# Optimization experiments

Hardware: AMD Instinct MI355X
Metric: run time of the kernel (lower is better)

## Reference

```python
import jax, jax.numpy as jnp
import numpy as np

N_NODES = 50000
N_EDGES = 800000
D_IN = 64
F1 = 64
F2 = 64
D_HID = 100


def setup_inputs() -> dict:
    key = jax.random.key(0)
    ks = jax.random.split(key, 12)
    x = jax.random.normal(ks[0], (N_NODES, D_IN), dtype=jnp.float32)
    edge_src = jax.random.randint(ks[1], (N_EDGES,), 0, N_NODES, dtype=jnp.int32)
    edge_dst = jax.random.randint(ks[2], (N_EDGES,), 0, N_NODES, dtype=jnp.int32)
    # stands in for pre-normalized GCN adjacency values (D^-1/2 (A+I) D^-1/2)
    edge_weight = jax.random.uniform(ks[3], (N_EDGES,), dtype=jnp.float32)
    def glorot(k, shape):
        lim = np.sqrt(6.0 / (shape[0] + shape[1]))
        return jax.random.uniform(k, shape, jnp.float32, -lim, lim)
    W1 = glorot(ks[4], (D_IN, F1))
    b1 = jnp.zeros((F1,), jnp.float32)
    W2 = glorot(ks[5], (F1, F2))
    b2 = jnp.zeros((F2,), jnp.float32)
    Wd = glorot(ks[6], (F2, D_HID))
    bd = jnp.zeros((D_HID,), jnp.float32)
    Wo = glorot(ks[7], (D_HID, 1))
    bo = jnp.zeros((1,), jnp.float32)
    return {"x": x, "edge_src": edge_src, "edge_dst": edge_dst,
            "edge_weight": edge_weight, "W1": W1, "b1": b1, "W2": W2,
            "b2": b2, "Wd": Wd, "bd": bd, "Wo": Wo, "bo": bo}


def _gcn_conv(x, edge_src, edge_dst, edge_weight, W, b):
    # spektral GCNConv: out = swish(A_norm @ (X @ W) + b)
    h = x @ W                                        # [N, F]
    msg = h[edge_src] * edge_weight[:, None]          # [E, F] gather + scale
    agg = jax.ops.segment_sum(msg, edge_dst, num_segments=N_NODES)  # [N, F]
    return jax.nn.swish(agg + b)


def reference(x, edge_src, edge_dst, edge_weight, W1, b1, W2, b2, Wd, bd, Wo, bo):
    h = _gcn_conv(x, edge_src, edge_dst, edge_weight, W1, b1)
    h = _gcn_conv(h, edge_src, edge_dst, edge_weight, W2, b2)
    h = jax.nn.swish(h @ Wd + bd)                    # Dense(100, swish)
    return jax.nn.sigmoid(h @ Wo + bo)               # Dense(1, sigmoid) -> [N, 1]
```

## Files before the change

### kernel.cpp

```cpp
#include <hip/hip_runtime.h>
#include <hip/hip_fp16.h>

#define N_NODES 50000
#define N_EDGES 800000
#define D 64
#define DHID 100
#define NTILES (N_NODES / 16)
#define NCT 7
#define CAP 32
#define SPILL_MAX 8192
#define NGROUPS 4
#define NSLICES 780
#define FILL_BLOCKS (NGROUPS * NSLICES)
#define MM_BLOCKS ((NTILES + 3) / 4)
#define DST_PER_GROUP (N_NODES / NGROUPS)
#define FSTRIDE (NSLICES * 256)
#define KMAX 5

typedef unsigned short ushort;
typedef unsigned int uint;
typedef __attribute__((ext_vector_type(8))) short s16x8;
typedef __attribute__((ext_vector_type(4))) float f32x4;

#define MFMA16(A, B, C) __builtin_amdgcn_mfma_f32_16x16x32_bf16((A), (B), (C), 0, 0, 0)

__device__ __forceinline__ float swishf(float x) { return x / (1.0f + __expf(-x)); }

__device__ __forceinline__ ushort f2bf(float f) {
    uint u = __float_as_uint(f);
    uint r = (u + 0x7fffu + ((u >> 16) & 1u)) >> 16;
    return (ushort)r;
}
__device__ __forceinline__ float bf2f(ushort h) { return __uint_as_float((uint)h << 16); }
__device__ __forceinline__ float bf_lo(uint d) { return __uint_as_float(d << 16); }
__device__ __forceinline__ float bf_hi(uint d) { return __uint_as_float(d & 0xffff0000u); }

__device__ __forceinline__ float hwf(uint e) {
    return __half2float(__ushort_as_half((ushort)(e >> 16)));
}

__device__ __forceinline__ void accum8(float* acc, uint4 v, float w) {
    acc[0] = fmaf(w, bf_lo(v.x), acc[0]);
    acc[1] = fmaf(w, bf_hi(v.x), acc[1]);
    acc[2] = fmaf(w, bf_lo(v.y), acc[2]);
    acc[3] = fmaf(w, bf_hi(v.y), acc[3]);
    acc[4] = fmaf(w, bf_lo(v.z), acc[4]);
    acc[5] = fmaf(w, bf_hi(v.z), acc[5]);
    acc[6] = fmaf(w, bf_lo(v.w), acc[6]);
    acc[7] = fmaf(w, bf_hi(v.w), acc[7]);
}

__device__ __forceinline__ void gather_body(const ushort* __restrict__ H,
                                            uint4 eA, uint4 eB, int degv,
                                            int j, int fg, float* acc) {
#pragma unroll
    for (int t = 0; t < 8; ++t) acc[t] = 0.f;
    const int sA = j * 4, sB = 16 + j * 4;
    bool pA = sA < degv, pB = sB < degv;
    uint4 vA0, vA1, vA2, vA3, vB0, vB1, vB2, vB3;
    float wA0 = 0, wA1 = 0, wA2 = 0, wA3 = 0;
    float wB0 = 0, wB1 = 0, wB2 = 0, wB3 = 0;
    if (pA) {
        wA0 = hwf(eA.x);
        wA1 = (sA + 1 < degv) ? hwf(eA.y) : 0.f;
        wA2 = (sA + 2 < degv) ? hwf(eA.z) : 0.f;
        wA3 = (sA + 3 < degv) ? hwf(eA.w) : 0.f;
        uint i0 = min(eA.x & 0xffffu, (uint)(N_NODES - 1));
        uint i1 = min(eA.y & 0xffffu, (uint)(N_NODES - 1));
        uint i2 = min(eA.z & 0xffffu, (uint)(N_NODES - 1));
        uint i3 = min(eA.w & 0xffffu, (uint)(N_NODES - 1));
        vA0 = *((const uint4*)(H + ((size_t)i0 << 6) + (fg << 3)));
        vA1 = *((const uint4*)(H + ((size_t)i1 << 6) + (fg << 3)));
        vA2 = *((const uint4*)(H + ((size_t)i2 << 6) + (fg << 3)));
        vA3 = *((const uint4*)(H + ((size_t)i3 << 6) + (fg << 3)));
    }
    if (pB) {
        wB0 = hwf(eB.x);
        wB1 = (sB + 1 < degv) ? hwf(eB.y) : 0.f;
        wB2 = (sB + 2 < degv) ? hwf(eB.z) : 0.f;
        wB3 = (sB + 3 < degv) ? hwf(eB.w) : 0.f;
        uint i0 = min(eB.x & 0xffffu, (uint)(N_NODES - 1));
        uint i1 = min(eB.y & 0xffffu, (uint)(N_NODES - 1));
        uint i2 = min(eB.z & 0xffffu, (uint)(N_NODES - 1));
        uint i3 = min(eB.w & 0xffffu, (uint)(N_NODES - 1));
        vB0 = *((const uint4*)(H + ((size_t)i0 << 6) + (fg << 3)));
        vB1 = *((const uint4*)(H + ((size_t)i1 << 6) + (fg << 3)));
        vB2 = *((const uint4*)(H + ((size_t)i2 << 6) + (fg << 3)));
        vB3 = *((const uint4*)(H + ((size_t)i3 << 6) + (fg << 3)));
    }
    if (pA) {
        accum8(acc, vA0, wA0);
        accum8(acc, vA1, wA1);
        accum8(acc, vA2, wA2);
        accum8(acc, vA3, wA3);
    }
    if (pB) {
        accum8(acc, vB0, wB0);
        accum8(acc, vB1, wB1);
        accum8(acc, vB2, wB2);
        accum8(acc, vB3, wB3);
    }
#pragma unroll
    for (int t = 0; t < 8; ++t) {
        acc[t] += __shfl_xor(acc[t], 8, 64);
        acc[t] += __shfl_xor(acc[t], 16, 64);
    }
}

__device__ __forceinline__ void add_spills(const ushort* __restrict__ H,
                                           const int* __restrict__ spillCnt,
                                           const uint2* __restrict__ spill,
                                           int node, int fg, float* acc) {
    int n = min(*spillCnt, SPILL_MAX);
    for (int i = 0; i < n; ++i) {
        uint2 sp = spill[i];
        if ((int)sp.x == node) {
            float wv = hwf(sp.y);
            uint si = min(sp.y & 0xffffu, (uint)(N_NODES - 1));
            uint4 v = *((const uint4*)(H + ((size_t)si << 6) + (fg << 3)));
            accum8(acc, v, wv);
        }
    }
}

__global__ __launch_bounds__(256) void fill_and_l1(const int* __restrict__ src,
                                                   const int* __restrict__ dst,
                                                   const float* __restrict__ w,
                                                   int* __restrict__ deg,
                                                   uint* __restrict__ csr,
                                                   int* __restrict__ spillCnt,
                                                   uint2* __restrict__ spill,
                                                   const float* __restrict__ X,
                                                   const float* __restrict__ W,
                                                   const float* __restrict__ W2,
                                                   const float* __restrict__ Wd,
                                                   short* __restrict__ W2T2,
                                                   short* __restrict__ WdT2,
                                                   ushort* __restrict__ H) {
    __shared__ __align__(16) short sBT[2][D][72];
    int tid = threadIdx.x;

    if (blockIdx.x < FILL_BLOCKS) {
        const int g = blockIdx.x & (NGROUPS - 1);
        const int s = blockIdx.x >> 2;
        const int lo = g * DST_PER_GROUP;
        const int e0 = s * 256 + tid;
        int d[KMAX];
        bool mk[KMAX];
#pragma unroll
        for (int k = 0; k < KMAX; ++k) {
            int e = e0 + k * FSTRIDE;
            int dv = (e < N_EDGES) ? dst[e] : -1;
            d[k] = dv;
            mk[k] = ((uint)(dv - lo) < (uint)DST_PER_GROUP);
        }
        float wv5[KMAX];
        int sv5[KMAX];
#pragma unroll
        for (int k = 0; k < KMAX; ++k)
            if (mk[k]) {
                int e = e0 + k * FSTRIDE;
                wv5[k] = __builtin_nontemporal_load(w + e);
                sv5[k] = __builtin_nontemporal_load(src + e);
            }
        int r5[KMAX];
#pragma unroll
        for (int k = 0; k < KMAX; ++k)
            if (mk[k]) r5[k] = atomicAdd(&deg[d[k]], 1);
#pragma unroll
        for (int k = 0; k < KMAX; ++k)
            if (mk[k]) {
                uint hw = (uint)__half_as_ushort(__float2half_rn(wv5[k]));
                uint payload = (uint)sv5[k] | (hw << 16);
                int r = r5[k];
                if (r < CAP) {
                    csr[(d[k] << 5) + r] = payload;
                } else {
                    int si = atomicAdd(spillCnt, 1);
                    if (si < SPILL_MAX) spill[si] = make_uint2((uint)d[k], payload);
                }
            }
        return;
    }

    if (blockIdx.x >= FILL_BLOCKS + MM_BLOCKS) {
        if (blockIdx.x == FILL_BLOCKS + MM_BLOCKS) {
            for (int idx = tid; idx < D * D; idx += 256) {
                int k = idx >> 6, c = idx & 63;
                float wv = W2[idx];
                ushort hi = f2bf(wv);
                W2T2[(size_t)c * D + k] = (short)hi;
                W2T2[(size_t)(D + c) * D + k] = (short)f2bf(wv - bf2f(hi));
            }
        } else {
            for (int idx = tid; idx < NCT * 16 * D; idx += 256) {
                int jj = idx >> 6, k = idx & 63;
                float wv = (jj < DHID) ? Wd[k * DHID + jj] : 0.f;
                ushort hi = f2bf(wv);
                WdT2[(size_t)jj * D + k] = (short)hi;
                WdT2[(size_t)(NCT * 16 + jj) * D + k] = (short)f2bf(wv - bf2f(hi));
            }
        }
        return;
    }

    for (int idx = tid; idx < D * D; idx += 256) {
        int k = idx >> 6, c = idx & 63;
        float wv = W[idx];
        ushort hi = f2bf(wv);
        sBT[0][c][k] = (short)hi;
        sBT[1][c][k] = (short)f2bf(wv - bf2f(hi));
    }
    __syncthreads();
    int wv_ = tid >> 6, lane = tid & 63, quad = lane >> 4, m = lane & 15;
    int tile = min((blockIdx.x - FILL_BLOCKS) * 4 + wv_, NTILES - 1);
    int node0 = tile * 16;

    f32x4 acc[4] = {{0,0,0,0},{0,0,0,0},{0,0,0,0},{0,0,0,0}};
#pragma unroll
    for (int kt = 0; kt < 2; ++kt) {
        int k0 = kt * 32 + quad * 8;
        const float* xp = X + ((size_t)(node0 + m) << 6) + k0;
        f32x4 xa = __builtin_nontemporal_load((const f32x4*)xp);
        f32x4 xb = __builtin_nontemporal_load((const f32x4*)(xp + 4));
        float xv[8] = {xa[0], xa[1], xa[2], xa[3], xb[0], xb[1], xb[2], xb[3]};
        s16x8 ahi, alo;
#pragma unroll
        for (int jj = 0; jj < 8; ++jj) {
            ushort hi = f2bf(xv[jj]);
            ahi[jj] = (short)hi;
            alo[jj] = (short)f2bf(xv[jj] - bf2f(hi));
        }
#pragma unroll
        for (int ct = 0; ct < 4; ++ct) {
            int n = ct * 16 + m;
            s16x8 bhi = *((const s16x8*)&sBT[0][n][k0]);
            s16x8 blo = *((const s16x8*)&sBT[1][n][k0]);
            acc[ct] = MFMA16(ahi, bhi, acc[ct]);
            acc[ct] = MFMA16(ahi, blo, acc[ct]);
            acc[ct] = MFMA16(alo, bhi, acc[ct]);
        }
    }
    __syncthreads();
    short (*rep)[16][72] = (short(*)[16][72])&sBT[0][0][0];
#pragma unroll
    for (int ct = 0; ct < 4; ++ct)
#pragma unroll
        for (int r = 0; r < 4; ++r)
            rep[wv_][quad * 4 + r][ct * 16 + m] = (short)f2bf(acc[ct][r]);
#pragma unroll
    for (int half = 0; half < 2; ++half) {
        int r = (lane >> 3) + half * 8;
        int c0 = (lane & 7) * 8;
        s16x8 v = *((const s16x8*)&rep[wv_][r][c0]);
        *((s16x8*)(H + ((size_t)(node0 + r) << 6) + c0)) = v;
    }
}

__global__ __launch_bounds__(256) void gather_act(const ushort* __restrict__ H,
                                                  const int* __restrict__ deg,
                                                  const uint* __restrict__ csr,
                                                  const int* __restrict__ spillCnt,
                                                  const uint2* __restrict__ spill,
                                                  const float* __restrict__ bias,
                                                  ushort* __restrict__ actOut) {
    int tid = threadIdx.x;
    int wave = tid >> 6, lane = tid & 63;
    int h = lane >> 5, j = (lane >> 3) & 3, fg = lane & 7;
    int node = blockIdx.x * 8 + wave * 2 + h;
    const uint* bucket = csr + ((size_t)node << 5);
    uint4 eA = *((const uint4*)(bucket + j * 4));
    uint4 eB = *((const uint4*)(bucket + 16 + j * 4));
    int degv = min(deg[node], CAP);

    float acc[8];
    gather_body(H, eA, eB, degv, j, fg, acc);
    if (j == 0) {
        add_spills(H, spillCnt, spill, node, fg, acc);
        float4 ba = ((const float4*)bias)[fg * 2];
        float4 bb = ((const float4*)bias)[fg * 2 + 1];
        float r0 = swishf(acc[0] + ba.x);
        float r1 = swishf(acc[1] + ba.y);
        float r2 = swishf(acc[2] + ba.z);
        float r3 = swishf(acc[3] + ba.w);
        float r4 = swishf(acc[4] + bb.x);
        float r5 = swishf(acc[5] + bb.y);
        float r6 = swishf(acc[6] + bb.z);
        float r7 = swishf(acc[7] + bb.w);
        uint4 u;
        u.x = (uint)f2bf(r0) | ((uint)f2bf(r1) << 16);
        u.y = (uint)f2bf(r2) | ((uint)f2bf(r3) << 16);
        u.z = (uint)f2bf(r4) | ((uint)f2bf(r5) << 16);
        u.w = (uint)f2bf(r6) | ((uint)f2bf(r7) << 16);
        *((uint4*)(actOut + ((size_t)node << 6) + (fg << 3))) = u;
    }
}

__global__ __launch_bounds__(256) void gather_tail(const ushort* __restrict__ act1,
                                                   const int* __restrict__ deg,
                                                   const uint* __restrict__ csr,
                                                   const int* __restrict__ spillCnt,
                                                   const uint2* __restrict__ spill,
                                                   const short* __restrict__ W2T2,
                                                   const float* __restrict__ b2,
                                                   const short* __restrict__ WdT2,
                                                   const float* __restrict__ bd,
                                                   const float* __restrict__ Wo,
                                                   const float* __restrict__ bo,
                                                   float* __restrict__ out) {
    __shared__ __align__(16) float sAgg[16][72];
    __shared__ __align__(16) short sAct2[16][72];
    __shared__ float sPart[4][16];
    int tid = threadIdx.x;
    int wv = tid >> 6, lane = tid & 63;
    int h = lane >> 5, j = (lane >> 3) & 3, fg = lane & 7;
    int quad = lane >> 4, m = lane & 15;
    int node0 = blockIdx.x * 16;

    {
        int n0l = wv * 4 + h, n1l = wv * 4 + 2 + h;
        int n0 = node0 + n0l, n1 = node0 + n1l;
        const uint* b0 = csr + ((size_t)n0 << 5);
        const uint* b1 = csr + ((size_t)n1 << 5);
        uint4 eA0 = *((const uint4*)(b0 + j * 4));
        uint4 eB0 = *((const uint4*)(b0 + 16 + j * 4));
        uint4 eA1 = *((const uint4*)(b1 + j * 4));
        uint4 eB1 = *((const uint4*)(b1 + 16 + j * 4));
        int d0 = min(deg[n0], CAP);
        int d1 = min(deg[n1], CAP);

        float acc0[8];
        gather_body(act1, eA0, eB0, d0, j, fg, acc0);
        if (j == 0) {
            add_spills(act1, spillCnt, spill, n0, fg, acc0);
            float4 u0 = {acc0[0], acc0[1], acc0[2], acc0[3]};
            float4 u1 = {acc0[4], acc0[5], acc0[6], acc0[7]};
            *((float4*)&sAgg[n0l][fg * 8]) = u0;
            *((float4*)&sAgg[n0l][fg * 8 + 4]) = u1;
        }
        float acc1[8];
        gather_body(act1, eA1, eB1, d1, j, fg, acc1);
        if (j == 0) {
            add_spills(act1, spillCnt, spill, n1, fg, acc1);
            float4 u0 = {acc1[0], acc1[1], acc1[2], acc1[3]};
            float4 u1 = {acc1[4], acc1[5], acc1[6], acc1[7]};
            *((float4*)&sAgg[n1l][fg * 8]) = u0;
            *((float4*)&sAgg[n1l][fg * 8 + 4]) = u1;
        }
    }
    __syncthreads();

    {
        f32x4 acc = {0, 0, 0, 0};
        int n = wv * 16 + m;
#pragma unroll
        for (int kt = 0; kt < 2; ++kt) {
            int k0 = kt * 32 + quad * 8;
            float4 xa = *((const float4*)&sAgg[m][k0]);
            float4 xb = *((const float4*)&sAgg[m][k0 + 4]);
            float xv[8] = {xa.x, xa.y, xa.z, xa.w, xb.x, xb.y, xb.z, xb.w};
            s16x8 ahi, alo;
#pragma unroll
            for (int jj = 0; jj < 8; ++jj) {
                ushort hi = f2bf(xv[jj]);
                ahi[jj] = (short)hi;
                alo[jj] = (short)f2bf(xv[jj] - bf2f(hi));
            }
            s16x8 bhi = *((const s16x8*)(W2T2 + (size_t)n * D + k0));
            s16x8 blo = *((const s16x8*)(W2T2 + (size_t)(D + n) * D + k0));
            acc = MFMA16(ahi, bhi, acc);
            acc = MFMA16(ahi, blo, acc);
            acc = MFMA16(alo, bhi, acc);
        }
        float bv = b2[n];
#pragma unroll
        for (int r = 0; r < 4; ++r)
            sAct2[quad * 4 + r][n] = (short)f2bf(swishf(acc[r] + bv));
    }
    __syncthreads();

    float part[4] = {0, 0, 0, 0};
#pragma unroll
    for (int cc = 0; cc < 2; ++cc) {
        int ct = wv + cc * 4;
        if (ct < NCT) {
            f32x4 acc = {0, 0, 0, 0};
            int n = ct * 16 + m;
#pragma unroll
            for (int kt = 0; kt < 2; ++kt) {
                int k0 = kt * 32 + quad * 8;
                s16x8 a = *((const s16x8*)&sAct2[m][k0]);
                s16x8 bhi = *((const s16x8*)(WdT2 + (size_t)n * D + k0));
                s16x8 blo = *((const s16x8*)(WdT2 + (size_t)(NCT * 16 + n) * D + k0));
                acc = MFMA16(a, bhi, acc);
                acc = MFMA16(a, blo, acc);
            }
            float bdv = (n < DHID) ? bd[n] : 0.f;
            float wov = (n < DHID) ? Wo[n] : 0.f;
#pragma unroll
            for (int r = 0; r < 4; ++r)
                part[r] = fmaf(swishf(acc[r] + bdv), wov, part[r]);
        }
    }
#pragma unroll
    for (int r = 0; r < 4; ++r) {
        part[r] += __shfl_xor(part[r], 1, 64);
        part[r] += __shfl_xor(part[r], 2, 64);
        part[r] += __shfl_xor(part[r], 4, 64);
        part[r] += __shfl_xor(part[r], 8, 64);
    }
    if (m == 0) {
#pragma unroll
        for (int r = 0; r < 4; ++r)
            sPart[wv][quad * 4 + r] = part[r];
    }
    __syncthreads();
    if (tid < 16) {
        float z = sPart[0][tid] + sPart[1][tid] + sPart[2][tid] + sPart[3][tid] + bo[0];
        out[node0 + tid] = 1.f / (1.f + __expf(-z));
    }
}

extern "C" void kernel_launch(void* const* d_in, const int* in_sizes, int n_in,
                              void* d_out, int out_size, void* d_ws, size_t ws_size,
                              hipStream_t stream) {
    const float* x   = (const float*)d_in[0];
    const int* esrc  = (const int*)d_in[1];
    const int* edst  = (const int*)d_in[2];
    const float* ew  = (const float*)d_in[3];
    const float* W1  = (const float*)d_in[4];
    const float* b1  = (const float*)d_in[5];
    const float* W2  = (const float*)d_in[6];
    const float* b2  = (const float*)d_in[7];
    const float* Wd  = (const float*)d_in[8];
    const float* bd  = (const float*)d_in[9];
    const float* Wo  = (const float*)d_in[10];
    const float* bo  = (const float*)d_in[11];
    float* out = (float*)d_out;

    char* ws = (char*)d_ws;
    ushort* H1    = (ushort*)ws; ws += (size_t)N_NODES * D * sizeof(ushort);
    ushort* act1  = (ushort*)ws; ws += (size_t)N_NODES * D * sizeof(ushort);
    uint* csr     = (uint*)ws;   ws += (size_t)N_NODES * CAP * sizeof(uint);
    int* deg      = (int*)ws;    ws += (size_t)N_NODES * sizeof(int);
    int* spillCnt = (int*)ws;    ws += 4 * sizeof(int);
    uint2* spill  = (uint2*)ws;  ws += (size_t)SPILL_MAX * sizeof(uint2);
    short* W2T2   = (short*)ws;  ws += (size_t)2 * D * D * sizeof(short);
    short* WdT2   = (short*)ws;  ws += (size_t)2 * NCT * 16 * D * sizeof(short);

    const int gBlocks = N_NODES / 8;

    hipMemsetAsync(deg, 0, (size_t)(N_NODES + 4) * sizeof(int), stream);

    fill_and_l1<<<FILL_BLOCKS + MM_BLOCKS + 2, 256, 0, stream>>>(
        esrc, edst, ew, deg, csr, spillCnt, spill, x, W1, W2, Wd, W2T2, WdT2, H1);

    gather_act<<<gBlocks, 256, 0, stream>>>(H1, deg, csr, spillCnt, spill, b1, act1);

    gather_tail<<<NTILES, 256, 0, stream>>>(act1, deg, csr, spillCnt, spill,
                                            W2T2, b2, WdT2, bd, Wo, bo, out);
}
```

Baseline: 179.7 us.

## Fuse three kernels into one persistent kernel with software grid barriers

Replaces the fill/L1, gather_act and gather_tail launches with one persistent kernel of 768 blocks. The phases are separated by atomic-counter grid barriers, and work is spread with grid-stride loops. This removes two kernel launch gaps and the tail effects between stages. In exchange, fewer blocks cover the scatter and gather phases, barrier spin cost is added, and correctness depends on all 768 blocks being resident at once.

```diff
diff --git a/kernel.cpp b/kernel.cpp
--- a/kernel.cpp
+++ b/kernel.cpp
@@ -10,12 +10,14 @@
 #define CAP 32
 #define SPILL_MAX 8192
 #define NGROUPS 4
-#define NSLICES 780
-#define FILL_BLOCKS (NGROUPS * NSLICES)
-#define MM_BLOCKS ((NTILES + 3) / 4)
 #define DST_PER_GROUP (N_NODES / NGROUPS)
-#define FSTRIDE (NSLICES * 256)
-#define KMAX 5
+#define NBLK 768
+#define NTHR 256
+#define GSIZE (NBLK * NTHR)
+#define FILLB 512
+#define L1B (NBLK - FILLB)
+#define FILL_NSL (FILLB / NGROUPS)
+#define FILL_STRIDE (FILL_NSL * NTHR)
 
 typedef unsigned short ushort;
 typedef unsigned int uint;
@@ -48,6 +50,28 @@
     acc[5] = fmaf(w, bf_hi(v.z), acc[5]);
     acc[6] = fmaf(w, bf_lo(v.w), acc[6]);
     acc[7] = fmaf(w, bf_hi(v.w), acc[7]);
+}
+
+struct GBar { uint cnt; uint gen; };
+
+__device__ __forceinline__ void gbar(GBar* b) {
+    __syncthreads();
+    if (threadIdx.x == 0) {
+        __threadfence();
+        uint g = atomicAdd(&b->gen, 0u);
+        uint v = atomicAdd(&b->cnt, 1u) + 1;
+        if (v == (uint)NBLK) {
+            atomicAdd(&b->gen, 1u);
+        } else {
+            int t = 0;
+            while (atomicAdd(&b->gen, 0u) == g) {
+                __builtin_amdgcn_s_sleep(8);
+                if (++t > 1000000) break;
+            }
+        }
+        __threadfence();
+    }
+    __syncthreads();
 }
 
 __device__ __forceinline__ void gather_body(const ushort* __restrict__ H,
@@ -123,301 +147,270 @@
     }
 }
 
-__global__ __launch_bounds__(256) void fill_and_l1(const int* __restrict__ src,
-                                                   const int* __restrict__ dst,
-                                                   const float* __restrict__ w,
-                                                   int* __restrict__ deg,
-                                                   uint* __restrict__ csr,
-                                                   int* __restrict__ spillCnt,
-                                                   uint2* __restrict__ spill,
-                                                   const float* __restrict__ X,
-                                                   const float* __restrict__ W,
-                                                   const float* __restrict__ W2,
-                                                   const float* __restrict__ Wd,
-                                                   short* __restrict__ W2T2,
-                                                   short* __restrict__ WdT2,
-                                                   ushort* __restrict__ H) {
+__global__ __launch_bounds__(NTHR, 4) void mega(const int* __restrict__ src,
+                                                const int* __restrict__ dst,
+                                                const float* __restrict__ w,
+                                                const float* __restrict__ X,
+                                                const float* __restrict__ W1,
+                                                const float* __restrict__ b1,
+                                                const float* __restrict__ W2,
+                                                const float* __restrict__ b2,
+                                                const float* __restrict__ Wd,
+                                                const float* __restrict__ bd,
+                                                const float* __restrict__ Wo,
+                                                const float* __restrict__ bo,
+                                                float* __restrict__ out,
+                                                int* __restrict__ deg,
+                                                uint* __restrict__ csr,
+                                                uint2* __restrict__ spill,
+                                                ushort* __restrict__ H1,
+                                                ushort* __restrict__ act1,
+                                                short* __restrict__ W2T2,
+                                                short* __restrict__ WdT2) {
     __shared__ __align__(16) short sBT[2][D][72];
-    int tid = threadIdx.x;
-
-    if (blockIdx.x < FILL_BLOCKS) {
-        const int g = blockIdx.x & (NGROUPS - 1);
-        const int s = blockIdx.x >> 2;
+    __shared__ __align__(16) char smemB[9216];
+    const int tid = threadIdx.x;
+    const int bid = blockIdx.x;
+    const int gtid = bid * NTHR + tid;
+    int* spillCnt = deg + N_NODES;
+    GBar* gb = (GBar*)(deg + N_NODES + 2);
+
+    for (int idx = gtid; idx < D * D; idx += GSIZE) {
+        int k = idx >> 6, c = idx & 63;
+        float wv = W2[idx];
+        ushort hi = f2bf(wv);
+        W2T2[(size_t)c * D + k] = (short)hi;
+        W2T2[(size_t)(D + c) * D + k] = (short)f2bf(wv - bf2f(hi));
+    }
+    for (int idx = gtid; idx < NCT * 16 * D; idx += GSIZE) {
+        int jj = idx >> 6, k = idx & 63;
+        float wv = (jj < DHID) ? Wd[k * DHID + jj] : 0.f;
+        ushort hi = f2bf(wv);
+        WdT2[(size_t)jj * D + k] = (short)hi;
+        WdT2[(size_t)(NCT * 16 + jj) * D + k] = (short)f2bf(wv - bf2f(hi));
+    }
+
+    if (bid < FILLB) {
+        const int g = bid & (NGROUPS - 1);
+        const int s = bid >> 2;
         const int lo = g * DST_PER_GROUP;
-        const int e0 = s * 256 + tid;
-        int d[KMAX];
-        bool mk[KMAX];
-#pragma unroll
-        for (int k = 0; k < KMAX; ++k) {
-            int e = e0 + k * FSTRIDE;
-            int dv = (e < N_EDGES) ? dst[e] : -1;
-            d[k] = dv;
-            mk[k] = ((uint)(dv - lo) < (uint)DST_PER_GROUP);
-        }
-        float wv5[KMAX];
-        int sv5[KMAX];
-#pragma unroll
-        for (int k = 0; k < KMAX; ++k)
-            if (mk[k]) {
-                int e = e0 + k * FSTRIDE;
-                wv5[k] = __builtin_nontemporal_load(w + e);
-                sv5[k] = __builtin_nontemporal_load(src + e);
-            }
-        int r5[KMAX];
-#pragma unroll
-        for (int k = 0; k < KMAX; ++k)
-            if (mk[k]) r5[k] = atomicAdd(&deg[d[k]], 1);
-#pragma unroll
-        for (int k = 0; k < KMAX; ++k)
-            if (mk[k]) {
-                uint hw = (uint)__half_as_ushort(__float2half_rn(wv5[k]));
-                uint payload = (uint)sv5[k] | (hw << 16);
-                int r = r5[k];
+#pragma unroll 2
+        for (int e = s * NTHR + tid; e < N_EDGES; e += FILL_STRIDE) {
+            int dv = dst[e];
+            if ((uint)(dv - lo) < (uint)DST_PER_GROUP) {
+                float wval = __builtin_nontemporal_load(w + e);
+                int sval = __builtin_nontemporal_load(src + e);
+                uint hw = (uint)__half_as_ushort(__float2half_rn(wval));
+                uint payload = (uint)sval | (hw << 16);
+                int r = atomicAdd(&deg[dv], 1);
                 if (r < CAP) {
-                    csr[(d[k] << 5) + r] = payload;
+                    csr[(dv << 5) + r] = payload;
                 } else {
                     int si = atomicAdd(spillCnt, 1);
-                    if (si < SPILL_MAX) spill[si] = make_uint2((uint)d[k], payload);
-                }
-            }
-        return;
-    }
-
-    if (blockIdx.x >= FILL_BLOCKS + MM_BLOCKS) {
-        if (blockIdx.x == FILL_BLOCKS + MM_BLOCKS) {
-            for (int idx = tid; idx < D * D; idx += 256) {
-                int k = idx >> 6, c = idx & 63;
-                float wv = W2[idx];
-                ushort hi = f2bf(wv);
-                W2T2[(size_t)c * D + k] = (short)hi;
-                W2T2[(size_t)(D + c) * D + k] = (short)f2bf(wv - bf2f(hi));
-            }
-        } else {
-            for (int idx = tid; idx < NCT * 16 * D; idx += 256) {
-                int jj = idx >> 6, k = idx & 63;
-                float wv = (jj < DHID) ? Wd[k * DHID + jj] : 0.f;
-                ushort hi = f2bf(wv);
-                WdT2[(size_t)jj * D + k] = (short)hi;
-                WdT2[(size_t)(NCT * 16 + jj) * D + k] = (short)f2bf(wv - bf2f(hi));
-            }
-        }
-        return;
-    }
-
-    for (int idx = tid; idx < D * D; idx += 256) {
-        int k = idx >> 6, c = idx & 63;
-        float wv = W[idx];
-        ushort hi = f2bf(wv);
-        sBT[0][c][k] = (short)hi;
-        sBT[1][c][k] = (short)f2bf(wv - bf2f(hi));
-    }
-    __syncthreads();
-    int wv_ = tid >> 6, lane = tid & 63, quad = lane >> 4, m = lane & 15;
-    int tile = min((blockIdx.x - FILL_BLOCKS) * 4 + wv_, NTILES - 1);
-    int node0 = tile * 16;
-
-    f32x4 acc[4] = {{0,0,0,0},{0,0,0,0},{0,0,0,0},{0,0,0,0}};
-#pragma unroll
-    for (int kt = 0; kt < 2; ++kt) {
-        int k0 = kt * 32 + quad * 8;
-        const float* xp = X + ((size_t)(node0 + m) << 6) + k0;
-        f32x4 xa = __builtin_nontemporal_load((const f32x4*)xp);
-        f32x4 xb = __builtin_nontemporal_load((const f32x4*)(xp + 4));
-        float xv[8] = {xa[0], xa[1], xa[2], xa[3], xb[0], xb[1], xb[2], xb[3]};
-        s16x8 ahi, alo;
-#pragma unroll
-        for (int jj = 0; jj < 8; ++jj) {
-            ushort hi = f2bf(xv[jj]);
-            ahi[jj] = (short)hi;
-            alo[jj] = (short)f2bf(xv[jj] - bf2f(hi));
-        }
-#pragma unroll
-        for (int ct = 0; ct < 4; ++ct) {
-            int n = ct * 16 + m;
-            s16x8 bhi = *((const s16x8*)&sBT[0][n][k0]);
-            s16x8 blo = *((const s16x8*)&sBT[1][n][k0]);
-            acc[ct] = MFMA16(ahi, bhi, acc[ct]);
-            acc[ct] = MFMA16(ahi, blo, acc[ct]);
-            acc[ct] = MFMA16(alo, bhi, acc[ct]);
-        }
-    }
-    __syncthreads();
-    short (*rep)[16][72] = (short(*)[16][72])&sBT[0][0][0];
-#pragma unroll
-    for (int ct = 0; ct < 4; ++ct)
-#pragma unroll
-        for (int r = 0; r < 4; ++r)
-            rep[wv_][quad * 4 + r][ct * 16 + m] = (short)f2bf(acc[ct][r]);
-#pragma unroll
-    for (int half = 0; half < 2; ++half) {
-        int r = (lane >> 3) + half * 8;
-        int c0 = (lane & 7) * 8;
-        s16x8 v = *((const s16x8*)&rep[wv_][r][c0]);
-        *((s16x8*)(H + ((size_t)(node0 + r) << 6) + c0)) = v;
-    }
-}
-
-__global__ __launch_bounds__(256) void gather_act(const ushort* __restrict__ H,
-                                                  const int* __restrict__ deg,
-                                                  const uint* __restrict__ csr,
-                                                  const int* __restrict__ spillCnt,
-                                                  const uint2* __restrict__ spill,
-                                                  const float* __restrict__ bias,
-                                                  ushort* __restrict__ actOut) {
-    int tid = threadIdx.x;
-    int wave = tid >> 6, lane = tid & 63;
-    int h = lane >> 5, j = (lane >> 3) & 3, fg = lane & 7;
-    int node = blockIdx.x * 8 + wave * 2 + h;
-    const uint* bucket = csr + ((size_t)node << 5);
-    uint4 eA = *((const uint4*)(bucket + j * 4));
-    uint4 eB = *((const uint4*)(bucket + 16 + j * 4));
-    int degv = min(deg[node], CAP);
-
-    float acc[8];
-    gather_body(H, eA, eB, degv, j, fg, acc);
-    if (j == 0) {
-        add_spills(H, spillCnt, spill, node, fg, acc);
-        float4 ba = ((const float4*)bias)[fg * 2];
-        float4 bb = ((const float4*)bias)[fg * 2 + 1];
-        float r0 = swishf(acc[0] + ba.x);
-        float r1 = swishf(acc[1] + ba.y);
-        float r2 = swishf(acc[2] + ba.z);
-        float r3 = swishf(acc[3] + ba.w);
-        float r4 = swishf(acc[4] + bb.x);
-        float r5 = swishf(acc[5] + bb.y);
-        float r6 = swishf(acc[6] + bb.z);
-        float r7 = swishf(acc[7] + bb.w);
-        uint4 u;
-        u.x = (uint)f2bf(r0) | ((uint)f2bf(r1) << 16);
-        u.y = (uint)f2bf(r2) | ((uint)f2bf(r3) << 16);
-        u.z = (uint)f2bf(r4) | ((uint)f2bf(r5) << 16);
-        u.w = (uint)f2bf(r6) | ((uint)f2bf(r7) << 16);
-        *((uint4*)(actOut + ((size_t)node << 6) + (fg << 3))) = u;
-    }
-}
-
-__global__ __launch_bounds__(256) void gather_tail(const ushort* __restrict__ act1,
-                                                   const int* __restrict__ deg,
-                                                   const uint* __restrict__ csr,
-                                                   const int* __restrict__ spillCnt,
-                                                   const uint2* __restrict__ spill,
-                                                   const short* __restrict__ W2T2,
-                                                   const float* __restrict__ b2,
-                                                   const short* __restrict__ WdT2,
-                                                   const float* __restrict__ bd,
-                                                   const float* __restrict__ Wo,
-                                                   const float* __restrict__ bo,
-                                                   float* __restrict__ out) {
-    __shared__ __align__(16) float sAgg[16][72];
-    __shared__ __align__(16) short sAct2[16][72];
-    __shared__ float sPart[4][16];
-    int tid = threadIdx.x;
-    int wv = tid >> 6, lane = tid & 63;
-    int h = lane >> 5, j = (lane >> 3) & 3, fg = lane & 7;
-    int quad = lane >> 4, m = lane & 15;
-    int node0 = blockIdx.x * 16;
-
-    {
-        int n0l = wv * 4 + h, n1l = wv * 4 + 2 + h;
-        int n0 = node0 + n0l, n1 = node0 + n1l;
-        const uint* b0 = csr + ((size_t)n0 << 5);
-        const uint* b1 = csr + ((size_t)n1 << 5);
-        uint4 eA0 = *((const uint4*)(b0 + j * 4));
-        uint4 eB0 = *((const uint4*)(b0 + 16 + j * 4));
-        uint4 eA1 = *((const uint4*)(b1 + j * 4));
-        uint4 eB1 = *((const uint4*)(b1 + 16 + j * 4));
-        int d0 = min(deg[n0], CAP);
-        int d1 = min(deg[n1], CAP);
-
-        float acc0[8];
-        gather_body(act1, eA0, eB0, d0, j, fg, acc0);
-        if (j == 0) {
-            add_spills(act1, spillCnt, spill, n0, fg, acc0);
-            float4 u0 = {acc0[0], acc0[1], acc0[2], acc0[3]};
-            float4 u1 = {acc0[4], acc0[5], acc0[6], acc0[7]};
-            *((float4*)&sAgg[n0l][fg * 8]) = u0;
-            *((float4*)&sAgg[n0l][fg * 8 + 4]) = u1;
-        }
-        float acc1[8];
-        gather_body(act1, eA1, eB1, d1, j, fg, acc1);
-        if (j == 0) {
-            add_spills(act1, spillCnt, spill, n1, fg, acc1);
-            float4 u0 = {acc1[0], acc1[1], acc1[2], acc1[3]};
-            float4 u1 = {acc1[4], acc1[5], acc1[6], acc1[7]};
-            *((float4*)&sAgg[n1l][fg * 8]) = u0;
-            *((float4*)&sAgg[n1l][fg * 8 + 4]) = u1;
-        }
-    }
-    __syncthreads();
-
-    {
-        f32x4 acc = {0, 0, 0, 0};
-        int n = wv * 16 + m;
-#pragma unroll
-        for (int kt = 0; kt < 2; ++kt) {
-            int k0 = kt * 32 + quad * 8;
-            float4 xa = *((const float4*)&sAgg[m][k0]);
-            float4 xb = *((const float4*)&sAgg[m][k0 + 4]);
-            float xv[8] = {xa.x, xa.y, xa.z, xa.w, xb.x, xb.y, xb.z, xb.w};
-            s16x8 ahi, alo;
-#pragma unroll
-            for (int jj = 0; jj < 8; ++jj) {
-                ushort hi = f2bf(xv[jj]);
-                ahi[jj] = (short)hi;
-                alo[jj] = (short)f2bf(xv[jj] - bf2f(hi));
-            }
-            s16x8 bhi = *((const s16x8*)(W2T2 + (size_t)n * D + k0));
-            s16x8 blo = *((const s16x8*)(W2T2 + (size_t)(D + n) * D + k0));
-            acc = MFMA16(ahi, bhi, acc);
-            acc = MFMA16(ahi, blo, acc);
-            acc = MFMA16(alo, bhi, acc);
-        }
-        float bv = b2[n];
-#pragma unroll
-        for (int r = 0; r < 4; ++r)
-            sAct2[quad * 4 + r][n] = (short)f2bf(swishf(acc[r] + bv));
-    }
-    __syncthreads();
-
-    float part[4] = {0, 0, 0, 0};
-#pragma unroll
-    for (int cc = 0; cc < 2; ++cc) {
-        int ct = wv + cc * 4;
-        if (ct < NCT) {
-            f32x4 acc = {0, 0, 0, 0};
-            int n = ct * 16 + m;
+                    if (si < SPILL_MAX) spill[si] = make_uint2((uint)dv, payload);
+                }
+            }
+        }
+    } else {
+        for (int idx = tid; idx < D * D; idx += NTHR) {
+            int k = idx >> 6, c = idx & 63;
+            float wv = W1[idx];
+            ushort hi = f2bf(wv);
+            sBT[0][c][k] = (short)hi;
+            sBT[1][c][k] = (short)f2bf(wv - bf2f(hi));
+        }
+        __syncthreads();
+        int wv_ = tid >> 6, lane = tid & 63, quad = lane >> 4, m = lane & 15;
+        short (*rep)[16][72] = (short(*)[16][72])smemB;
+        for (int slot = (bid - FILLB) * 4 + wv_; slot < NTILES; slot += L1B * 4) {
+            int node0 = slot * 16;
+            f32x4 acc[4] = {{0,0,0,0},{0,0,0,0},{0,0,0,0},{0,0,0,0}};
 #pragma unroll
             for (int kt = 0; kt < 2; ++kt) {
                 int k0 = kt * 32 + quad * 8;
-                s16x8 a = *((const s16x8*)&sAct2[m][k0]);
-                s16x8 bhi = *((const s16x8*)(WdT2 + (size_t)n * D + k0));
-                s16x8 blo = *((const s16x8*)(WdT2 + (size_t)(NCT * 16 + n) * D + k0));
-                acc = MFMA16(a, bhi, acc);
-                acc = MFMA16(a, blo, acc);
-            }
-            float bdv = (n < DHID) ? bd[n] : 0.f;
-            float wov = (n < DHID) ? Wo[n] : 0.f;
-#pragma unroll
-            for (int r = 0; r < 4; ++r)
-                part[r] = fmaf(swishf(acc[r] + bdv), wov, part[r]);
-        }
-    }
-#pragma unroll
-    for (int r = 0; r < 4; ++r) {
-        part[r] += __shfl_xor(part[r], 1, 64);
-        part[r] += __shfl_xor(part[r], 2, 64);
-        part[r] += __shfl_xor(part[r], 4, 64);
-        part[r] += __shfl_xor(part[r], 8, 64);
-    }
-    if (m == 0) {
-#pragma unroll
-        for (int r = 0; r < 4; ++r)
-            sPart[wv][quad * 4 + r] = part[r];
-    }
-    __syncthreads();
-    if (tid < 16) {
-        float z = sPart[0][tid] + sPart[1][tid] + sPart[2][tid] + sPart[3][tid] + bo[0];
-        out[node0 + tid] = 1.f / (1.f + __expf(-z));
+                const float* xp = X + ((size_t)(node0 + m) << 6) + k0;
+                f32x4 xa = __builtin_nontemporal_load((const f32x4*)xp);
+                f32x4 xb = __builtin_nontemporal_load((const f32x4*)(xp + 4));
+                float xv[8] = {xa[0], xa[1], xa[2], xa[3], xb[0], xb[1], xb[2], xb[3]};
+                s16x8 ahi, alo;
+#pragma unroll
+                for (int jj = 0; jj < 8; ++jj) {
+                    ushort hi = f2bf(xv[jj]);
+                    ahi[jj] = (short)hi;
+                    alo[jj] = (short)f2bf(xv[jj] - bf2f(hi));
+                }
+#pragma unroll
+                for (int ct = 0; ct < 4; ++ct) {
+                    int n = ct * 16 + m;
+                    s16x8 bhi = *((const s16x8*)&sBT[0][n][k0]);
+                    s16x8 blo = *((const s16x8*)&sBT[1][n][k0]);
+                    acc[ct] = MFMA16(ahi, bhi, acc[ct]);
+                    acc[ct] = MFMA16(ahi, blo, acc[ct]);
+                    acc[ct] = MFMA16(alo, bhi, acc[ct]);
+                }
+            }
+#pragma unroll
+            for (int ct = 0; ct < 4; ++ct)
+#pragma unroll
+                for (int r = 0; r < 4; ++r)
+                    rep[wv_][quad * 4 + r][ct * 16 + m] = (short)f2bf(acc[ct][r]);
+#pragma unroll
+            for (int half = 0; half < 2; ++half) {
+                int r = (lane >> 3) + half * 8;
+                int c0 = (lane & 7) * 8;
+                s16x8 v = *((const s16x8*)&rep[wv_][r][c0]);
+                *((s16x8*)(H1 + ((size_t)(node0 + r) << 6) + c0)) = v;
+            }
+        }
+    }
+    gbar(&gb[0]);
+
+    {
+        int wave = tid >> 6, lane = tid & 63;
+        int h = lane >> 5, j = (lane >> 3) & 3, fg = lane & 7;
+        for (int u = bid; u < N_NODES / 8; u += NBLK) {
+            int node = u * 8 + wave * 2 + h;
+            const uint* bucket = csr + ((size_t)node << 5);
+            uint4 eA = *((const uint4*)(bucket + j * 4));
+            uint4 eB = *((const uint4*)(bucket + 16 + j * 4));
+            int degv = min(deg[node], CAP);
+            float acc[8];
+            gather_body(H1, eA, eB, degv, j, fg, acc);
+            if (j == 0) {
+                add_spills(H1, spillCnt, spill, node, fg, acc);
+                float4 ba = ((const float4*)b1)[fg * 2];
+                float4 bb = ((const float4*)b1)[fg * 2 + 1];
+                float r0 = swishf(acc[0] + ba.x);
+                float r1 = swishf(acc[1] + ba.y);
+                float r2 = swishf(acc[2] + ba.z);
+                float r3 = swishf(acc[3] + ba.w);
+                float r4 = swishf(acc[4] + bb.x);
+                float r5 = swishf(acc[5] + bb.y);
+                float r6 = swishf(acc[6] + bb.z);
+                float r7 = swishf(acc[7] + bb.w);
+                uint4 u4;
+                u4.x = (uint)f2bf(r0) | ((uint)f2bf(r1) << 16);
+                u4.y = (uint)f2bf(r2) | ((uint)f2bf(r3) << 16);
+                u4.z = (uint)f2bf(r4) | ((uint)f2bf(r5) << 16);
+                u4.w = (uint)f2bf(r6) | ((uint)f2bf(r7) << 16);
+                *((uint4*)(act1 + ((size_t)node << 6) + (fg << 3))) = u4;
+            }
+        }
+    }
+    gbar(&gb[1]);
+
+    {
+        float (*sAgg)[72] = (float(*)[72])smemB;
+        short (*sAct2)[72] = (short(*)[72])(smemB + 4608);
+        float (*sPart)[16] = (float(*)[16])(smemB + 6912);
+        int wv = tid >> 6, lane = tid & 63;
+        int h = lane >> 5, j = (lane >> 3) & 3, fg = lane & 7;
+        int quad = lane >> 4, m = lane & 15;
+        for (int t = bid; t < NTILES; t += NBLK) {
+            int node0 = t * 16;
+            {
+                int n0l = wv * 4 + h, n1l = wv * 4 + 2 + h;
+                int n0 = node0 + n0l, n1 = node0 + n1l;
+                const uint* bk0 = csr + ((size_t)n0 << 5);
+                const uint* bk1 = csr + ((size_t)n1 << 5);
+                uint4 eA0 = *((const uint4*)(bk0 + j * 4));
+                uint4 eB0 = *((const uint4*)(bk0 + 16 + j * 4));
+                uint4 eA1 = *((const uint4*)(bk1 + j * 4));
+                uint4 eB1 = *((const uint4*)(bk1 + 16 + j * 4));
+                int d0 = min(deg[n0], CAP);
+                int d1 = min(deg[n1], CAP);
+                float acc0[8];
+                gather_body(act1, eA0, eB0, d0, j, fg, acc0);
+                if (j == 0) {
+                    add_spills(act1, spillCnt, spill, n0, fg, acc0);
+                    float4 u0 = {acc0[0], acc0[1], acc0[2], acc0[3]};
+                    float4 u1 = {acc0[4], acc0[5], acc0[6], acc0[7]};
+                    *((float4*)&sAgg[n0l][fg * 8]) = u0;
+                    *((float4*)&sAgg[n0l][fg * 8 + 4]) = u1;
+                }
+                float acc1[8];
+                gather_body(act1, eA1, eB1, d1, j, fg, acc1);
+                if (j == 0) {
+                    add_spills(act1, spillCnt, spill, n1, fg, acc1);
+                    float4 u0 = {acc1[0], acc1[1], acc1[2], acc1[3]};
+                    float4 u1 = {acc1[4], acc1[5], acc1[6], acc1[7]};
+                    *((float4*)&sAgg[n1l][fg * 8]) = u0;
+                    *((float4*)&sAgg[n1l][fg * 8 + 4]) = u1;
+                }
+            }
+            __syncthreads();
+
+            {
+                f32x4 acc = {0, 0, 0, 0};
+                int n = wv * 16 + m;
+#pragma unroll
+                for (int kt = 0; kt < 2; ++kt) {
+                    int k0 = kt * 32 + quad * 8;
+                    float4 xa = *((const float4*)&sAgg[m][k0]);
+                    float4 xb = *((const float4*)&sAgg[m][k0 + 4]);
+                    float xv[8] = {xa.x, xa.y, xa.z, xa.w, xb.x, xb.y, xb.z, xb.w};
+                    s16x8 ahi, alo;
+#pragma unroll
+                    for (int jj = 0; jj < 8; ++jj) {
+                        ushort hi = f2bf(xv[jj]);
+                        ahi[jj] = (short)hi;
+                        alo[jj] = (short)f2bf(xv[jj] - bf2f(hi));
+                    }
+                    s16x8 bhi = *((const s16x8*)(W2T2 + (size_t)n * D + k0));
+                    s16x8 blo = *((const s16x8*)(W2T2 + (size_t)(D + n) * D + k0));
+                    acc = MFMA16(ahi, bhi, acc);
+                    acc = MFMA16(ahi, blo, acc);
+                    acc = MFMA16(alo, bhi, acc);
+                }
+                float bv = b2[n];
+#pragma unroll
+                for (int r = 0; r < 4; ++r)
+                    sAct2[quad * 4 + r][n] = (short)f2bf(swishf(acc[r] + bv));
+            }
+            __syncthreads();
+
+            float part[4] = {0, 0, 0, 0};
+#pragma unroll
+            for (int cc = 0; cc < 2; ++cc) {
+                int ct = wv + cc * 4;
+                if (ct < NCT) {
+                    f32x4 acc = {0, 0, 0, 0};
+                    int n = ct * 16 + m;
+#pragma unroll
+                    for (int kt = 0; kt < 2; ++kt) {
+                        int k0 = kt * 32 + quad * 8;
+                        s16x8 a = *((const s16x8*)&sAct2[m][k0]);
+                        s16x8 bhi = *((const s16x8*)(WdT2 + (size_t)n * D + k0));
+                        s16x8 blo = *((const s16x8*)(WdT2 + (size_t)(NCT * 16 + n) * D + k0));
+                        acc = MFMA16(a, bhi, acc);
+                        acc = MFMA16(a, blo, acc);
+                    }
+                    float bdv = (n < DHID) ? bd[n] : 0.f;
+                    float wov = (n < DHID) ? Wo[n] : 0.f;
+#pragma unroll
+                    for (int r = 0; r < 4; ++r)
+                        part[r] = fmaf(swishf(acc[r] + bdv), wov, part[r]);
+                }
+            }
+#pragma unroll
+            for (int r = 0; r < 4; ++r) {
+                part[r] += __shfl_xor(part[r], 1, 64);
+                part[r] += __shfl_xor(part[r], 2, 64);
+                part[r] += __shfl_xor(part[r], 4, 64);
+                part[r] += __shfl_xor(part[r], 8, 64);
+            }
+            if (m == 0) {
+#pragma unroll
+                for (int r = 0; r < 4; ++r)
+                    sPart[wv][quad * 4 + r] = part[r];
+            }
+            __syncthreads();
+            if (tid < 16) {
+                float z = sPart[0][tid] + sPart[1][tid] + sPart[2][tid] + sPart[3][tid] + bo[0];
+                out[node0 + tid] = 1.f / (1.f + __expf(-z));
+            }
+            __syncthreads();
+        }
     }
 }
 
@@ -442,21 +435,14 @@
     ushort* H1    = (ushort*)ws; ws += (size_t)N_NODES * D * sizeof(ushort);
     ushort* act1  = (ushort*)ws; ws += (size_t)N_NODES * D * sizeof(ushort);
     uint* csr     = (uint*)ws;   ws += (size_t)N_NODES * CAP * sizeof(uint);
-    int* deg      = (int*)ws;    ws += (size_t)N_NODES * sizeof(int);
-    int* spillCnt = (int*)ws;    ws += 4 * sizeof(int);
+    int* deg      = (int*)ws;    ws += (size_t)(N_NODES + 8) * sizeof(int);
     uint2* spill  = (uint2*)ws;  ws += (size_t)SPILL_MAX * sizeof(uint2);
     short* W2T2   = (short*)ws;  ws += (size_t)2 * D * D * sizeof(short);
     short* WdT2   = (short*)ws;  ws += (size_t)2 * NCT * 16 * D * sizeof(short);
 
-    const int gBlocks = N_NODES / 8;
-
-    hipMemsetAsync(deg, 0, (size_t)(N_NODES + 4) * sizeof(int), stream);
-
-    fill_and_l1<<<FILL_BLOCKS + MM_BLOCKS + 2, 256, 0, stream>>>(
-        esrc, edst, ew, deg, csr, spillCnt, spill, x, W1, W2, Wd, W2T2, WdT2, H1);
-
-    gather_act<<<gBlocks, 256, 0, stream>>>(H1, deg, csr, spillCnt, spill, b1, act1);
-
-    gather_tail<<<NTILES, 256, 0, stream>>>(act1, deg, csr, spillCnt, spill,
-                                            W2T2, b2, WdT2, bd, Wo, bo, out);
-}
+    hipMemsetAsync(deg, 0, (size_t)(N_NODES + 8) * sizeof(int), stream);
+
+    mega<<<NBLK, NTHR, 0, stream>>>(esrc, edst, ew, x, W1, b1, W2, b2, Wd, bd,
+                                    Wo, bo, out, deg, csr, spill, H1, act1,
+                                    W2T2, WdT2);
+}
```

After: 416.0 us. +131.5%, slower.
